# Kernel tuning notes

Measured on AMD Instinct MI355X. Metric: run time of the kernel, lower is better.

The kernel has to match this reference:

```python
import jax, jax.numpy as jnp
import numpy as np

B, U, SIZE, D_ATT = 8, 1024, 1024, 1024
NEG_INF = -1e38


def setup_inputs() -> dict:
    key = jax.random.key(0)
    ks = jax.random.split(key, 16)
    s = 0.02
    return {
        "x": jax.random.normal(ks[0], (B, U, SIZE), jnp.float32),
        "time_decay": jax.random.normal(ks[1], (D_ATT,), jnp.float32),
        "time_first": jax.random.normal(ks[2], (D_ATT,), jnp.float32),
        "time_mix_key": jax.random.uniform(ks[3], (1, 1, SIZE), jnp.float32),
        "time_mix_value": jax.random.uniform(ks[4], (1, 1, SIZE), jnp.float32),
        "time_mix_receptance": jax.random.uniform(ks[5], (1, 1, SIZE), jnp.float32),
        "W_key": jax.random.normal(ks[6], (SIZE, D_ATT), jnp.float32) * s,
        "b_key": jax.random.normal(ks[7], (D_ATT,), jnp.float32) * s,
        "W_value": jax.random.normal(ks[8], (SIZE, D_ATT), jnp.float32) * s,
        "b_value": jax.random.normal(ks[9], (D_ATT,), jnp.float32) * s,
        "W_receptance": jax.random.normal(ks[10], (SIZE, D_ATT), jnp.float32) * s,
        "b_receptance": jax.random.normal(ks[11], (D_ATT,), jnp.float32) * s,
        "W_output": jax.random.normal(ks[12], (D_ATT, SIZE), jnp.float32) * s,
        "b_output": jax.random.normal(ks[13], (SIZE,), jnp.float32) * s,
    }


def wkv_scan(time_decay, time_first, k, v):
    """Numerically-stable RWKV WKV recurrence. k, v: (B, U, D)."""
    w = -jnp.exp(time_decay)  # (D,)

    def step(carry, kv):
        a, b, p = carry  # each (B, D): numerator, denominator, running max
        kt, vt = kv      # (B, D)
        # output at step t (includes time_first bonus for current token)
        q = jnp.maximum(p, time_first + kt)
        e1 = jnp.exp(p - q)
        e2 = jnp.exp(time_first + kt - q)
        out = (e1 * a + e2 * vt) / (e1 * b + e2)
        # state update (decay by w)
        q2 = jnp.maximum(p + w, kt)
        e1 = jnp.exp(p + w - q2)
        e2 = jnp.exp(kt - q2)
        return (e1 * a + e2 * vt, e1 * b + e2, q2), out

    Bb, Uu, Dd = k.shape
    init = (
        jnp.zeros((Bb, Dd), k.dtype),
        jnp.zeros((Bb, Dd), k.dtype),
        jnp.full((Bb, Dd), NEG_INF, k.dtype),
    )
    _, out = jax.lax.scan(step, init, (k.transpose(1, 0, 2), v.transpose(1, 0, 2)))
    return out.transpose(1, 0, 2)  # (B, U, D)


def reference(x, time_decay, time_first, time_mix_key, time_mix_value,
              time_mix_receptance, W_key, b_key, W_value, b_value,
              W_receptance, b_receptance, W_output, b_output):
    # time_shift: shifted[t] = x[t-1], shifted[0] = 0
    shifted = jnp.pad(x, ((0, 0), (1, 0), (0, 0)))[:, :-1, :]
    k_in = x * time_mix_key + shifted * (1.0 - time_mix_key)
    v_in = x * time_mix_value + shifted * (1.0 - time_mix_value)
    r_in = x * time_mix_receptance + shifted * (1.0 - time_mix_receptance)
    k = jnp.einsum("bus,sd->bud", k_in, W_key) + b_key
    v = jnp.einsum("bus,sd->bud", v_in, W_value) + b_value
    r = jax.nn.sigmoid(jnp.einsum("bus,sd->bud", r_in, W_receptance) + b_receptance)
    wkv = wkv_scan(time_decay, time_first, k, v)
    out = jnp.einsum("bud,ds->bus", r * wkv, W_output) + b_output
    return out
```

## Files before the change

kernel.cpp:

```cpp
#include <hip/hip_runtime.h>
#include <cstdint>
#include <cstddef>

#define B_DIM 8
#define U_DIM 1024
#define SD    1024
#define M_DIM (B_DIM * U_DIM)
#define NC 32
#define CT 32

typedef __attribute__((ext_vector_type(8))) short short8;
typedef __attribute__((ext_vector_type(4))) float f32x4;

typedef __attribute__((address_space(3))) void       lds_t;
typedef const __attribute__((address_space(1))) void glb_t;

__device__ __forceinline__ ushort f2bf(float f) {
    union { float f; uint32_t u; } c; c.f = f;
    uint32_t r = (c.u + 0x7FFFu + ((c.u >> 16) & 1u)) >> 16;
    return (ushort)r;
}
__device__ __forceinline__ float bf2f(ushort h) {
    union { float f; uint32_t u; } c; c.u = ((uint32_t)h) << 16; return c.f;
}

__global__ __launch_bounds__(256)
void wtrans_kernel(const float* __restrict__ Wk, const float* __restrict__ Wv,
                   const float* __restrict__ Wr, const float* __restrict__ Wo,
                   ushort* __restrict__ WT)
{
    __shared__ float t[32][33];
    const float* W = (blockIdx.z == 0) ? Wk : (blockIdx.z == 1) ? Wv
                   : (blockIdx.z == 2) ? Wr : Wo;
    ushort* o = WT + (size_t)blockIdx.z * SD * SD;
    const int tx = threadIdx.x & 31, ty = threadIdx.x >> 5;
    const int k0 = blockIdx.y * 32, n0 = blockIdx.x * 32;
    #pragma unroll
    for (int i = 0; i < 4; ++i)
        t[ty + i * 8][tx] = W[(size_t)(k0 + ty + i * 8) * SD + n0 + tx];
    __syncthreads();
    #pragma unroll
    for (int i = 0; i < 4; ++i)
        o[(size_t)(n0 + ty + i * 8) * SD + k0 + tx] = f2bf(t[tx][ty + i * 8]);
}

__global__ __launch_bounds__(256)
void mix3_kernel(const float* __restrict__ x,
                 const float* __restrict__ mk, const float* __restrict__ mv,
                 const float* __restrict__ mr,
                 ushort* __restrict__ Ak, ushort* __restrict__ Av,
                 ushort* __restrict__ Ar)
{
    const int idx = blockIdx.x * 256 + threadIdx.x;
    const int m = idx >> 8;
    const int s = (idx & 255) << 2;
    const float4 xv = *(const float4*)&x[(size_t)m * SD + s];
    float4 sh = make_float4(0.f, 0.f, 0.f, 0.f);
    if (m & (U_DIM - 1)) sh = *(const float4*)&x[(size_t)(m - 1) * SD + s];
    const float4 dx = make_float4(xv.x - sh.x, xv.y - sh.y, xv.z - sh.z, xv.w - sh.w);
    const size_t off = (size_t)m * SD + s;

    float4 mx;
    ushort4 o;
    mx = *(const float4*)&mk[s];
    o.x = f2bf(sh.x + mx.x * dx.x); o.y = f2bf(sh.y + mx.y * dx.y);
    o.z = f2bf(sh.z + mx.z * dx.z); o.w = f2bf(sh.w + mx.w * dx.w);
    *(ushort4*)&Ak[off] = o;
    mx = *(const float4*)&mv[s];
    o.x = f2bf(sh.x + mx.x * dx.x); o.y = f2bf(sh.y + mx.y * dx.y);
    o.z = f2bf(sh.z + mx.z * dx.z); o.w = f2bf(sh.w + mx.w * dx.w);
    *(ushort4*)&Av[off] = o;
    mx = *(const float4*)&mr[s];
    o.x = f2bf(sh.x + mx.x * dx.x); o.y = f2bf(sh.y + mx.y * dx.y);
    o.z = f2bf(sh.z + mx.z * dx.z); o.w = f2bf(sh.w + mx.w * dx.w);
    *(ushort4*)&Ar[off] = o;
}

__global__ __launch_bounds__(256)
void mix_kernel(const float* __restrict__ x, const float* __restrict__ mix,
                ushort* __restrict__ outA)
{
    const int idx = blockIdx.x * 256 + threadIdx.x;
    const int m = idx >> 8;
    const int s = (idx & 255) << 2;
    const float4 xv = *(const float4*)&x[(size_t)m * SD + s];
    float4 sh = make_float4(0.f, 0.f, 0.f, 0.f);
    if (m & (U_DIM - 1)) sh = *(const float4*)&x[(size_t)(m - 1) * SD + s];
    const float4 mx = *(const float4*)&mix[s];
    ushort4 o;
    o.x = f2bf(sh.x + mx.x * (xv.x - sh.x));
    o.y = f2bf(sh.y + mx.y * (xv.y - sh.y));
    o.z = f2bf(sh.z + mx.z * (xv.z - sh.z));
    o.w = f2bf(sh.w + mx.w * (xv.w - sh.w));
    *(ushort4*)&outA[(size_t)m * SD + s] = o;
}

template<int FUSED>
__global__ __launch_bounds__(256)
void gemm128(const ushort* __restrict__ Abase, const ushort* __restrict__ WTbase,
             const float* __restrict__ b0, const float* __restrict__ b1,
             const float* __restrict__ b2, void* __restrict__ Cbase)
{
    __shared__ ushort As[128 * 32];
    __shared__ ushort Bs[128 * 32];

    const int tid = threadIdx.x;
    const int wv = tid >> 6, ln = tid & 63;
    const int wm = (wv >> 1) * 64, wn = (wv & 1) * 64;

    const int m0 = blockIdx.x * 128;
    int nb = (int)blockIdx.y, z = 0;
    if (FUSED == 3) { z = nb >> 3; nb &= 7; }
    const int n0 = nb * 128;

    const ushort* A; const ushort* BT; const float* bias; void* Cout; int dosig;
    if (FUSED == 3) {
        A    = Abase + (size_t)z * ((size_t)M_DIM * SD);
        BT   = WTbase + (size_t)z * ((size_t)SD * SD);
        bias = (z == 0) ? b0 : (z == 1) ? b1 : b2;
        Cout = (void*)((ushort*)Cbase + (size_t)z * ((size_t)M_DIM * SD));
        dosig = (z == 2);
    } else {
        A = Abase; BT = WTbase; bias = b0; Cout = Cbase; dosig = (FUSED == 1);
    }

    const int srow = tid >> 2;
    const int sq   = ((tid & 3) ^ ((srow >> 1) & 3)) << 3;
    const ushort* aS = A  + (size_t)(m0 + srow) * SD + sq;
    const ushort* bS = BT + (size_t)(n0 + srow) * SD + sq;
    char* const laW = (char*)As + wv * 1024;
    char* const lbW = (char*)Bs + wv * 1024;

    const int lr  = ln & 15;
    const int lq  = ln >> 4;
    const int kof = (lq ^ ((lr >> 1) & 3)) << 4;
    const char* LAc = (const char*)As;
    const char* LBc = (const char*)Bs;
    const int aRd = wm * 64 + lr * 64 + kof;
    const int bRd = wn * 64 + lr * 64 + kof;

    f32x4 acc[4][4];
    #pragma unroll
    for (int i = 0; i < 4; ++i)
        #pragma unroll
        for (int j = 0; j < 4; ++j)
            acc[i][j] = (f32x4){0.f, 0.f, 0.f, 0.f};

    for (int k0 = 0; k0 < SD; k0 += 32) {
        __builtin_amdgcn_global_load_lds((glb_t*)(aS + k0),                 (lds_t*)laW,          16, 0, 0);
        __builtin_amdgcn_global_load_lds((glb_t*)(aS + (size_t)64 * SD + k0), (lds_t*)(laW + 4096), 16, 0, 0);
        __builtin_amdgcn_global_load_lds((glb_t*)(bS + k0),                 (lds_t*)lbW,          16, 0, 0);
        __builtin_amdgcn_global_load_lds((glb_t*)(bS + (size_t)64 * SD + k0), (lds_t*)(lbW + 4096), 16, 0, 0);
        __syncthreads();

        short8 af[4], bq[4];
        #pragma unroll
        for (int mt = 0; mt < 4; ++mt)
            af[mt] = *(const short8*)(LAc + mt * 1024 + aRd);
        #pragma unroll
        for (int nt = 0; nt < 4; ++nt)
            bq[nt] = *(const short8*)(LBc + nt * 1024 + bRd);
        #pragma unroll
        for (int mt = 0; mt < 4; ++mt)
            #pragma unroll
            for (int nt = 0; nt < 4; ++nt)
                acc[mt][nt] = __builtin_amdgcn_mfma_f32_16x16x32_bf16(
                    af[mt], bq[nt], acc[mt][nt], 0, 0, 0);
        __syncthreads();
    }

    const int cr = lq * 4;
    const int cc = lr;
    #pragma unroll
    for (int mt = 0; mt < 4; ++mt)
    #pragma unroll
    for (int nt = 0; nt < 4; ++nt) {
        const int gc = n0 + wn + nt * 16 + cc;
        const float bv = bias[gc];
        #pragma unroll
        for (int j = 0; j < 4; ++j) {
            const int gr = m0 + wm + mt * 16 + cr + j;
            float v = acc[mt][nt][j] + bv;
            if (FUSED == 1 || FUSED == 3) { if (dosig) v = 1.f / (1.f + __expf(-v)); }
            if (FUSED == 2)
                ((float*)Cout)[(size_t)gr * SD + gc] = v;
            else
                ((ushort*)Cout)[(size_t)gr * SD + gc] = f2bf(v);
        }
    }
}

__global__ __launch_bounds__(256)
void scan_local(const ushort* __restrict__ kq, const ushort* __restrict__ vq,
                const float* __restrict__ td,
                float* __restrict__ sa, float* __restrict__ sb, float* __restrict__ sp)
{
    const int idx = blockIdx.x * 256 + threadIdx.x;
    const int ch = idx & (M_DIM - 1);
    const int c  = idx >> 13;
    const int b  = ch >> 10, d = ch & (SD - 1);
    const float w = -__expf(td[d]);
    size_t ptr = (size_t)b * U_DIM * SD + (size_t)(c * CT) * SD + d;

    float a = 0.f, bb = 0.f, p = -1e38f;
    for (int s = 0; s < CT; ++s) {
        const float kt = bf2f(kq[ptr]), vt = bf2f(vq[ptr]);
        const float q2 = fmaxf(p + w, kt);
        const float e1 = __expf(p + w - q2);
        const float e2 = __expf(kt - q2);
        a = e1 * a + e2 * vt; bb = e1 * bb + e2; p = q2;
        ptr += SD;
    }
    sa[idx] = a; sb[idx] = bb; sp[idx] = p;
}

__global__ __launch_bounds__(256)
void scan_prefix(const float* __restrict__ td,
                 float* __restrict__ sa, float* __restrict__ sb, float* __restrict__ sp)
{
    const int ch = blockIdx.x * 256 + threadIdx.x;
    const float wT = -__expf(td[ch & (SD - 1)]) * (float)CT;
    float ca = 0.f, cb = 0.f, cp = -1e38f;
    for (int c = 0; c < NC; ++c) {
        const int i = c * M_DIM + ch;
        const float la = sa[i], lb = sb[i], lp = sp[i];
        sa[i] = ca; sb[i] = cb; sp[i] = cp;
        const float pd = cp + wT;
        const float q  = fmaxf(pd, lp);
        const float e1 = __expf(pd - q);
        const float e2 = __expf(lp - q);
        ca = e1 * ca + e2 * la; cb = e1 * cb + e2 * lb; cp = q;
    }
}

__global__ __launch_bounds__(256)
void scan_out(const ushort* __restrict__ kq, const ushort* __restrict__ vq,
              const ushort* __restrict__ rq,
              const float* __restrict__ td, const float* __restrict__ tfirst,
              const float* __restrict__ sa, const float* __restrict__ sb,
              const float* __restrict__ sp,
              ushort* __restrict__ rw)
{
    const int idx = blockIdx.x * 256 + threadIdx.x;
    const int ch = idx & (M_DIM - 1);
    const int c  = idx >> 13;
    const int b  = ch >> 10, d = ch & (SD - 1);
    const float w  = -__expf(td[d]);
    const float tf = tfirst[d];
    size_t ptr = (size_t)b * U_DIM * SD + (size_t)(c * CT) * SD + d;

    float a = sa[idx], bb = sb[idx], p = sp[idx];
    for (int s = 0; s < CT; ++s) {
        const float kt = bf2f(kq[ptr]), vt = bf2f(vq[ptr]), rt = bf2f(rq[ptr]);
        const float q  = fmaxf(p, tf + kt);
        const float e1 = __expf(p - q);
        const float e2 = __expf(tf + kt - q);
        const float ov = (e1 * a + e2 * vt) * __builtin_amdgcn_rcpf(e1 * bb + e2);
        const float q2  = fmaxf(p + w, kt);
        const float e1b = __expf(p + w - q2);
        const float e2b = __expf(kt - q2);
        a = e1b * a + e2b * vt; bb = e1b * bb + e2b; p = q2;
        rw[ptr] = f2bf(rt * ov);
        ptr += SD;
    }
}

extern "C" void kernel_launch(void* const* d_in, const int* in_sizes, int n_in,
                              void* d_out, int out_size, void* d_ws, size_t ws_size,
                              hipStream_t stream)
{
    (void)in_sizes; (void)n_in; (void)out_size;
    const float* x  = (const float*)d_in[0];
    const float* td = (const float*)d_in[1];
    const float* tf = (const float*)d_in[2];
    const float* mk = (const float*)d_in[3];
    const float* mv = (const float*)d_in[4];
    const float* mr = (const float*)d_in[5];
    const float* Wk = (const float*)d_in[6];
    const float* bk = (const float*)d_in[7];
    const float* Wv = (const float*)d_in[8];
    const float* bv = (const float*)d_in[9];
    const float* Wr = (const float*)d_in[10];
    const float* br = (const float*)d_in[11];
    const float* Wo = (const float*)d_in[12];
    const float* bo = (const float*)d_in[13];
    float* out = (float*)d_out;

    const size_t NE = (size_t)M_DIM * SD;
    const size_t WS = (size_t)SD * SD;
    char* ws = (char*)d_ws;

    const dim3 gg1(64, 8, 1);
    const dim3 gg3(64, 24, 1);

    if (ws_size >= ((size_t)108 << 20)) {
        ushort* WT  = (ushort*)ws;
        ushort* Ak  = (ushort*)(ws + ((size_t)8   << 20));
        ushort* kvr = (ushort*)(ws + ((size_t)56  << 20));
        float*  sa  = (float*)(ws + ((size_t)104 << 20));
        float*  sb  = (float*)(ws + ((size_t)105 << 20));
        float*  sp  = (float*)(ws + ((size_t)106 << 20));
        ushort* kbuf = kvr;
        ushort* vbuf = kvr + NE;
        ushort* rbuf = kvr + 2 * NE;
        ushort* rwkv = Ak;

        wtrans_kernel<<<dim3(32, 32, 4), 256, 0, stream>>>(Wk, Wv, Wr, Wo, WT);
        mix3_kernel<<<8192, 256, 0, stream>>>(x, mk, mv, mr, Ak, Ak + NE, Ak + 2 * NE);
        gemm128<3><<<gg3, 256, 0, stream>>>(Ak, WT, bk, bv, br, kvr);

        scan_local <<<(M_DIM * NC) / 256, 256, 0, stream>>>(kbuf, vbuf, td, sa, sb, sp);
        scan_prefix<<<M_DIM / 256, 256, 0, stream>>>(td, sa, sb, sp);
        scan_out   <<<(M_DIM * NC) / 256, 256, 0, stream>>>(kbuf, vbuf, rbuf, td, tf,
                                                            sa, sb, sp, rwkv);

        gemm128<2><<<gg1, 256, 0, stream>>>(rwkv, WT + 3 * WS, bo, bo, bo, out);
    } else {
        ushort* WT   = (ushort*)ws;
        ushort* Abuf = (ushort*)(ws + ((size_t)8  << 20));
        ushort* kbuf = (ushort*)(ws + ((size_t)24 << 20));
        ushort* vbuf = (ushort*)(ws + ((size_t)40 << 20));
        ushort* rbuf = (ushort*)(ws + ((size_t)56 << 20));
        float*  sa   = (float*)(ws + ((size_t)72 << 20));
        float*  sb   = (float*)(ws + ((size_t)73 << 20));
        float*  sp   = (float*)(ws + ((size_t)74 << 20));
        ushort* rwkv = Abuf;

        wtrans_kernel<<<dim3(32, 32, 4), 256, 0, stream>>>(Wk, Wv, Wr, Wo, WT);
        mix_kernel<<<8192, 256, 0, stream>>>(x, mk, Abuf);
        gemm128<0><<<gg1, 256, 0, stream>>>(Abuf, WT, bk, bk, bk, kbuf);
        mix_kernel<<<8192, 256, 0, stream>>>(x, mv, Abuf);
        gemm128<0><<<gg1, 256, 0, stream>>>(Abuf, WT + WS, bv, bv, bv, vbuf);
        mix_kernel<<<8192, 256, 0, stream>>>(x, mr, Abuf);
        gemm128<1><<<gg1, 256, 0, stream>>>(Abuf, WT + 2 * WS, br, br, br, rbuf);

        scan_local <<<(M_DIM * NC) / 256, 256, 0, stream>>>(kbuf, vbuf, td, sa, sb, sp);
        scan_prefix<<<M_DIM / 256, 256, 0, stream>>>(td, sa, sb, sp);
        scan_out   <<<(M_DIM * NC) / 256, 256, 0, stream>>>(kbuf, vbuf, rbuf, td, tf,
                                                            sa, sb, sp, rwkv);

        gemm128<2><<<gg1, 256, 0, stream>>>(rwkv, WT + 3 * WS, bo, bo, bo, out);
    }
}
```

Measured before the change: 148.3 us.

## Stage GEMM epilogue through LDS for coalesced stores and remap workgroups to XCDs

The GEMM epilogue now writes the bias-added (and optionally sigmoid) results into shared memory in passes, then writes them back with 16-byte row-contiguous vector stores instead of scattered 2- or 4-byte stores. The block index is also remapped so that consecutive workgroups spread across the eight XCDs, with neighbouring M tiles sharing an N panel, to improve L2 reuse of weight panels. The A and B tiles now share a single LDS buffer that is reused for output staging. The extra barriers in the epilogue add some synchronisation cost, and the remap assumes the grid x dimension is 64.

```diff
diff --git a/kernel.cpp b/kernel.cpp
--- a/kernel.cpp
+++ b/kernel.cpp
@@ -101,16 +101,20 @@
              const float* __restrict__ b0, const float* __restrict__ b1,
              const float* __restrict__ b2, void* __restrict__ Cbase)
 {
-    __shared__ ushort As[128 * 32];
-    __shared__ ushort Bs[128 * 32];
+    __shared__ ushort SMEM[8192];
 
     const int tid = threadIdx.x;
     const int wv = tid >> 6, ln = tid & 63;
     const int wm = (wv >> 1) * 64, wn = (wv & 1) * 64;
 
-    const int m0 = blockIdx.x * 128;
-    int nb = (int)blockIdx.y, z = 0;
-    if (FUSED == 3) { z = nb >> 3; nb &= 7; }
+    const int nwg = (int)(gridDim.x * gridDim.y);
+    const int bid = (int)blockIdx.x + 64 * (int)blockIdx.y;
+    const int s_  = (bid & 7) * (nwg >> 3) + (bid >> 3);
+    const int mb  = s_ & 63;
+    const int pan = s_ >> 6;
+    const int m0 = mb * 128;
+    int nb = pan, z = 0;
+    if (FUSED == 3) { nb = pan & 7; z = pan >> 3; }
     const int n0 = nb * 128;
 
     const ushort* A; const ushort* BT; const float* bias; void* Cout; int dosig;
@@ -128,14 +132,14 @@
     const int sq   = ((tid & 3) ^ ((srow >> 1) & 3)) << 3;
     const ushort* aS = A  + (size_t)(m0 + srow) * SD + sq;
     const ushort* bS = BT + (size_t)(n0 + srow) * SD + sq;
-    char* const laW = (char*)As + wv * 1024;
-    char* const lbW = (char*)Bs + wv * 1024;
+    char* const laW = (char*)SMEM + wv * 1024;
+    char* const lbW = (char*)(SMEM + 4096) + wv * 1024;
 
     const int lr  = ln & 15;
     const int lq  = ln >> 4;
     const int kof = (lq ^ ((lr >> 1) & 3)) << 4;
-    const char* LAc = (const char*)As;
-    const char* LBc = (const char*)Bs;
+    const char* LAc = (const char*)SMEM;
+    const char* LBc = (const char*)(SMEM + 4096);
     const int aRd = wm * 64 + lr * 64 + kof;
     const int bRd = wn * 64 + lr * 64 + kof;
 
@@ -147,9 +151,9 @@
             acc[i][j] = (f32x4){0.f, 0.f, 0.f, 0.f};
 
     for (int k0 = 0; k0 < SD; k0 += 32) {
-        __builtin_amdgcn_global_load_lds((glb_t*)(aS + k0),                 (lds_t*)laW,          16, 0, 0);
+        __builtin_amdgcn_global_load_lds((glb_t*)(aS + k0),                   (lds_t*)laW,          16, 0, 0);
         __builtin_amdgcn_global_load_lds((glb_t*)(aS + (size_t)64 * SD + k0), (lds_t*)(laW + 4096), 16, 0, 0);
-        __builtin_amdgcn_global_load_lds((glb_t*)(bS + k0),                 (lds_t*)lbW,          16, 0, 0);
+        __builtin_amdgcn_global_load_lds((glb_t*)(bS + k0),                   (lds_t*)lbW,          16, 0, 0);
         __builtin_amdgcn_global_load_lds((glb_t*)(bS + (size_t)64 * SD + k0), (lds_t*)(lbW + 4096), 16, 0, 0);
         __syncthreads();
 
@@ -171,21 +175,63 @@
 
     const int cr = lq * 4;
     const int cc = lr;
-    #pragma unroll
-    for (int mt = 0; mt < 4; ++mt)
-    #pragma unroll
-    for (int nt = 0; nt < 4; ++nt) {
-        const int gc = n0 + wn + nt * 16 + cc;
-        const float bv = bias[gc];
-        #pragma unroll
-        for (int j = 0; j < 4; ++j) {
-            const int gr = m0 + wm + mt * 16 + cr + j;
-            float v = acc[mt][nt][j] + bv;
-            if (FUSED == 1 || FUSED == 3) { if (dosig) v = 1.f / (1.f + __expf(-v)); }
-            if (FUSED == 2)
-                ((float*)Cout)[(size_t)gr * SD + gc] = v;
-            else
-                ((ushort*)Cout)[(size_t)gr * SD + gc] = f2bf(v);
+    if (FUSED != 2) {
+        ushort* Cu = (ushort*)Cout;
+        #pragma unroll
+        for (int pass = 0; pass < 2; ++pass) {
+            if ((wv >> 1) == pass) {
+                #pragma unroll
+                for (int mt = 0; mt < 4; ++mt)
+                #pragma unroll
+                for (int nt = 0; nt < 4; ++nt) {
+                    const int gcL = wn + nt * 16 + cc;
+                    const float bv = bias[n0 + gcL];
+                    #pragma unroll
+                    for (int j = 0; j < 4; ++j) {
+                        float v = acc[mt][nt][j] + bv;
+                        if (dosig) v = 1.f / (1.f + __expf(-v));
+                        SMEM[(mt * 16 + cr + j) * 128 + gcL] = f2bf(v);
+                    }
+                }
+            }
+            __syncthreads();
+            #pragma unroll
+            for (int it = 0; it < 4; ++it) {
+                const int row = it * 16 + (tid >> 4);
+                const int co  = (tid & 15) * 8;
+                *(short8*)&Cu[(size_t)(m0 + pass * 64 + row) * SD + n0 + co] =
+                    *(const short8*)&SMEM[row * 128 + co];
+            }
+            __syncthreads();
+        }
+    } else {
+        float* Cf = (float*)Cout;
+        float* fS = (float*)SMEM;
+        #pragma unroll
+        for (int pass = 0; pass < 4; ++pass) {
+            if ((wv >> 1) == (pass >> 1)) {
+                #pragma unroll
+                for (int mt2 = 0; mt2 < 2; ++mt2) {
+                    const int mt = (pass & 1) * 2 + mt2;
+                    #pragma unroll
+                    for (int nt = 0; nt < 4; ++nt) {
+                        const int gcL = wn + nt * 16 + cc;
+                        const float bv = bias[n0 + gcL];
+                        #pragma unroll
+                        for (int j = 0; j < 4; ++j)
+                            fS[(mt2 * 16 + cr + j) * 128 + gcL] = acc[mt][nt][j] + bv;
+                    }
+                }
+            }
+            __syncthreads();
+            #pragma unroll
+            for (int it = 0; it < 4; ++it) {
+                const int row = it * 8 + (tid >> 5);
+                const int co  = (tid & 31) * 4;
+                *(float4*)&Cf[(size_t)(m0 + pass * 32 + row) * SD + n0 + co] =
+                    *(const float4*)&fS[row * 128 + co];
+            }
+            __syncthreads();
         }
     }
 }
```

After: 169.5 us. +14.3%, slower.
